# Kernel tuning notes

Measured on AMD Instinct MI355X. Metric: run time of the kernel, lower is better.

## Reference

```python
import jax, jax.numpy as jnp
import numpy as np

N = 50000
E = 800000
DIN = 256
DH = 256
DOUT = 256
R = 8
B = 4


def setup_inputs() -> dict:
    key = jax.random.key(0)
    ks = jax.random.split(key, 12)
    s = 0.05
    return {
        "x": jax.random.normal(ks[0], (N, DIN), jnp.float32),
        "edge_index": jax.random.randint(ks[1], (2, E), 0, N, jnp.int64),
        "edge_type": jax.random.randint(ks[2], (E,), 0, R, jnp.int64),
        "basis1": jax.random.normal(ks[3], (B, DIN, DH), jnp.float32) * s,
        "comp1": jax.random.normal(ks[4], (R, B), jnp.float32) * s,
        "root1": jax.random.normal(ks[5], (DIN, DH), jnp.float32) * s,
        "bias1": jnp.zeros((DH,), jnp.float32),
        "basis2": jax.random.normal(ks[6], (B, DH, DOUT), jnp.float32) * s,
        "comp2": jax.random.normal(ks[7], (R, B), jnp.float32) * s,
        "root2": jax.random.normal(ks[8], (DH, DOUT), jnp.float32) * s,
        "bias2": jnp.zeros((DOUT,), jnp.float32),
    }


def rgcn_conv(x, src, dst, edge_type, basis, comp, root, bias):
    # Basis-decomposed relational conv (PyG RGCNConv, aggr='mean').
    # xb: per-node transform by each basis matrix -> [N, B, out]
    xb = jnp.einsum('ni,bio->nbo', x, basis)
    # Per-edge message: mix bases with relation coefficients -> [E, out]
    msg = jnp.einsum('eb,ebo->eo', comp[edge_type], xb[src])
    # Mean aggregation per (dst, relation): divide each edge by the count of
    # edges of its relation arriving at its destination, then scatter-add.
    key = dst * R + edge_type
    cnt = jax.ops.segment_sum(jnp.ones((msg.shape[0],), x.dtype), key,
                              num_segments=x.shape[0] * R)
    norm = 1.0 / jnp.maximum(cnt, 1.0)
    agg = jax.ops.segment_sum(msg * norm[key][:, None], dst,
                              num_segments=x.shape[0])
    return agg + x @ root + bias


def reference(x, edge_index, edge_type, basis1, comp1, root1, bias1,
              basis2, comp2, root2, bias2):
    src, dst = edge_index[0], edge_index[1]
    h = rgcn_conv(x, src, dst, edge_type, basis1, comp1, root1, bias1)
    h = jax.nn.relu(h)
    # dropout(p=0.4) is identity in eval mode
    out = rgcn_conv(h, src, dst, edge_type, basis2, comp2, root2, bias2)
    return out
```

## Files before the change

kernel.cpp:

```cpp
#include <hip/hip_runtime.h>
#include <hip/hip_bf16.h>

constexpr int N_NODES = 50000;
constexpr int N_EDGES = 800000;
constexpr int R_REL   = 8;
constexpr int BASES   = 4;
constexpr int D       = 256;
constexpr int KT      = BASES * D + D;

typedef __attribute__((ext_vector_type(8))) short bf16x8;
typedef __attribute__((ext_vector_type(4))) float f32x4;

__device__ inline float bfu_lo(unsigned u) { return __uint_as_float(u << 16); }
__device__ inline float bfu_hi(unsigned u) { return __uint_as_float(u & 0xFFFF0000u); }
__device__ inline unsigned short f2bu(float f) {
  __hip_bfloat16 h = __float2bfloat16(f);
  return *reinterpret_cast<unsigned short*>(&h);
}
__device__ inline void store_out(float* p, float v) { *p = v; }
__device__ inline void store_out(__hip_bfloat16* p, float v) { *p = __float2bfloat16(v); }

__device__ inline void gload_lds16(void* lds, const void* g) {
  __builtin_amdgcn_global_load_lds(
      (const __attribute__((address_space(1))) unsigned*)g,
      (__attribute__((address_space(3))) unsigned*)lds, 16, 0, 0);
}

__global__ __launch_bounds__(256) void count_kernel(
    const int* __restrict__ ei, const int* __restrict__ et,
    int* __restrict__ cnt) {
  int e = blockIdx.x * 256 + threadIdx.x;
  if (e < N_EDGES) {
    int dst = ei[N_EDGES + e];
    int rt  = et[e];
    atomicAdd(&cnt[dst * R_REL + rt], 1);
  }
}

__global__ __launch_bounds__(256) void scan_phaseA(
    const int* __restrict__ cnt, int* __restrict__ bsum) {
  __shared__ int sd[256];
  int tid = threadIdx.x;
  int n = blockIdx.x * 256 + tid;
  int d = 0;
  if (n < N_NODES) {
#pragma unroll
    for (int r = 0; r < R_REL; r++) d += cnt[n * R_REL + r];
  }
  sd[tid] = d;
  __syncthreads();
  for (int off = 128; off > 0; off >>= 1) {
    if (tid < off) sd[tid] += sd[tid + off];
    __syncthreads();
  }
  if (tid == 0) bsum[blockIdx.x] = sd[0];
}

__global__ __launch_bounds__(256) void scan_phaseB(
    const int* __restrict__ bsum, int* __restrict__ boff,
    int* __restrict__ estart, int NB) {
  __shared__ int sd[256];
  int tid = threadIdx.x;
  int v = (tid < NB) ? bsum[tid] : 0;
  sd[tid] = v;
  __syncthreads();
  for (int off = 1; off < 256; off <<= 1) {
    int t = (tid >= off) ? sd[tid - off] : 0;
    __syncthreads();
    sd[tid] += t;
    __syncthreads();
  }
  if (tid < NB) boff[tid] = sd[tid] - v;
  if (tid == 0) estart[N_NODES] = N_EDGES;
}

__global__ __launch_bounds__(256) void scan_phaseC(
    const int* __restrict__ cnt, const int* __restrict__ boff,
    int* __restrict__ estart) {
  __shared__ int sd[256];
  int tid = threadIdx.x;
  int n = blockIdx.x * 256 + tid;
  int d = 0;
  if (n < N_NODES) {
#pragma unroll
    for (int r = 0; r < R_REL; r++) d += cnt[n * R_REL + r];
  }
  sd[tid] = d;
  __syncthreads();
  for (int off = 1; off < 256; off <<= 1) {
    int t = (tid >= off) ? sd[tid - off] : 0;
    __syncthreads();
    sd[tid] += t;
    __syncthreads();
  }
  if (n < N_NODES) estart[n] = boff[blockIdx.x] + sd[tid] - d;
}

__global__ __launch_bounds__(256) void bucket_kernel(
    const int* __restrict__ ei, const int* __restrict__ et,
    const int* __restrict__ estart, int* __restrict__ cursor,
    int* __restrict__ packed) {
  int e = blockIdx.x * 256 + threadIdx.x;
  if (e < N_EDGES) {
    int src = ei[e];
    int dst = ei[N_EDGES + e];
    int rt  = et[e];
    int pos = estart[dst] + atomicAdd(&cursor[dst], 1);
    packed[pos] = src | (rt << 20);
  }
}

__global__ __launch_bounds__(256) void convert_kernel(
    const float* __restrict__ x, unsigned* __restrict__ x2) {
  int idx = blockIdx.x * 256 + threadIdx.x;
  if (idx < N_NODES * 128) {
    float2 v = *(const float2*)(x + (size_t)idx * 2);
    x2[idx] = (unsigned)f2bu(v.x) | ((unsigned)f2bu(v.y) << 16);
  }
}

__global__ __launch_bounds__(256) void winv_kernel(
    const int* __restrict__ cnt, const float* __restrict__ comp,
    float4* __restrict__ wtab) {
  int idx = blockIdx.x * 256 + threadIdx.x;
  if (idx < N_NODES * R_REL) {
    int r = idx & 7;
    int c = cnt[idx];
    float inv = 1.0f / (float)(c > 0 ? c : 1);
    float4 w;
    w.x = comp[r * BASES + 0] * inv;
    w.y = comp[r * BASES + 1] * inv;
    w.z = comp[r * BASES + 2] * inv;
    w.w = comp[r * BASES + 3] * inv;
    wtab[idx] = w;
  }
}

__global__ __launch_bounds__(256) void make_w_kernel(
    const float* __restrict__ basis, const float* __restrict__ root,
    __hip_bfloat16* __restrict__ WT) {
  __shared__ __hip_bfloat16 tile[64][256];
  int k0 = blockIdx.x * 64;
  int tid = threadIdx.x;
#pragma unroll 4
  for (int r = 0; r < 64; r++) {
    int k = k0 + r;
    const float* srow = (k < BASES * D)
        ? basis + ((size_t)(k & 3) * D + (k >> 2)) * D
        : root + (size_t)(k - BASES * D) * D;
    tile[r][tid] = __float2bfloat16(srow[tid]);
  }
  __syncthreads();
  __hip_bfloat16* dst = WT + (size_t)tid * KT + k0;
#pragma unroll
  for (int c = 0; c < 8; c++) {
    union { short s[8]; int4 v; } u;
#pragma unroll
    for (int r = 0; r < 8; r++)
      u.s[r] = *reinterpret_cast<short*>(&tile[c * 8 + r][tid]);
    *(int4*)(dst + c * 8) = u.v;
  }
}

__device__ inline void edge_fma(float acc[BASES][4], uint2 v, float4 w) {
  float a0 = bfu_lo(v.x), a1 = bfu_hi(v.x), a2 = bfu_lo(v.y), a3 = bfu_hi(v.y);
  acc[0][0] += w.x * a0; acc[0][1] += w.x * a1; acc[0][2] += w.x * a2; acc[0][3] += w.x * a3;
  acc[1][0] += w.y * a0; acc[1][1] += w.y * a1; acc[1][2] += w.y * a2; acc[1][3] += w.y * a3;
  acc[2][0] += w.z * a0; acc[2][1] += w.z * a1; acc[2][2] += w.z * a2; acc[2][3] += w.z * a3;
  acc[3][0] += w.w * a0; acc[3][1] += w.w * a1; acc[3][2] += w.w * a2; acc[3][3] += w.w * a3;
}

__global__ __launch_bounds__(256) void aggregate_kernel(
    const unsigned* __restrict__ x2,
    const int* __restrict__ packed,
    const int* __restrict__ estart,
    const float4* __restrict__ wtab,
    __hip_bfloat16* __restrict__ zA)
{
  int tid = threadIdx.x;
  int wave = tid >> 6, lane = tid & 63;
  int n = blockIdx.x * 4 + wave;
  const float4 wzero = make_float4(0.f, 0.f, 0.f, 0.f);

  float acc[BASES][4] = {};
  int s = estart[n], e = estart[n + 1];
  const float4* wt = wtab + (size_t)n * R_REL;

  for (int base = s; base < e; base += 4) {
    int rem = e - base;
    int i1 = base + (rem > 1 ? 1 : 0);
    int i2 = base + (rem > 2 ? 2 : 0);
    int i3 = base + (rem > 3 ? 3 : 0);
    int p0 = packed[base];
    int p1 = packed[i1];
    int p2 = packed[i2];
    int p3 = packed[i3];
    uint2 v0 = *(const uint2*)(x2 + (size_t)(p0 & 0xFFFFF) * 128 + lane * 2);
    uint2 v1 = *(const uint2*)(x2 + (size_t)(p1 & 0xFFFFF) * 128 + lane * 2);
    uint2 v2 = *(const uint2*)(x2 + (size_t)(p2 & 0xFFFFF) * 128 + lane * 2);
    uint2 v3 = *(const uint2*)(x2 + (size_t)(p3 & 0xFFFFF) * 128 + lane * 2);
    float4 w0 = wt[p0 >> 20];
    float4 w1 = (rem > 1) ? wt[p1 >> 20] : wzero;
    float4 w2 = (rem > 2) ? wt[p2 >> 20] : wzero;
    float4 w3 = (rem > 3) ? wt[p3 >> 20] : wzero;
    edge_fma(acc, v0, w0);
    edge_fma(acc, v1, w1);
    edge_fma(acc, v2, w2);
    edge_fma(acc, v3, w3);
  }

  union { short s[8]; int4 v; } u0, u1;
#pragma unroll
  for (int j = 0; j < 2; j++)
#pragma unroll
    for (int b = 0; b < BASES; b++) {
      u0.s[4 * j + b] = (short)f2bu(acc[b][j]);
      u1.s[4 * j + b] = (short)f2bu(acc[b][j + 2]);
    }
  __hip_bfloat16* zrow = zA + (size_t)n * KT;
  *(int4*)(zrow + 16 * lane) = u0.v;
  *(int4*)(zrow + 16 * lane + 8) = u1.v;

  uint2 sv = *(const uint2*)(x2 + (size_t)n * 128 + lane * 2);
  *(uint2*)((unsigned*)(zrow + BASES * D) + lane * 2) = sv;
}

#define BM 128
#define BN 256
#define BK 32

template <bool RELU, typename OutT>
__global__ __launch_bounds__(512) void gemm_kernel(
    const __hip_bfloat16* __restrict__ A,
    const __hip_bfloat16* __restrict__ Bt,
    const float* __restrict__ bias, OutT* __restrict__ C, int M) {
  __shared__ __align__(16) __hip_bfloat16 As[BM * BK];
  __shared__ __align__(16) __hip_bfloat16 Bs[BN * BK];
  int tid = threadIdx.x;
  int m0 = blockIdx.x * BM;
  int wave = tid >> 6, lane = tid & 63;
  int wm = wave & 1, wn = wave >> 1;
  int l15 = lane & 15, quad = lane >> 4;

  int colS = (lane & 3) * 8;
  int rowA = wave * 16 + (lane >> 2);
  int grA  = min(m0 + rowA, M - 1);
  const __hip_bfloat16* gA  = A + (size_t)grA * KT + colS;
  const __hip_bfloat16* gB0 = Bt + (size_t)(wave * 32 + (lane >> 2)) * KT + colS;
  const __hip_bfloat16* gB1 = gB0 + 16 * KT;
  __hip_bfloat16* lA  = As + wave * 512;
  __hip_bfloat16* lB0 = Bs + wave * 1024;
  __hip_bfloat16* lB1 = Bs + wave * 1024 + 512;

  f32x4 acc[4][4] = {};

  for (int k0 = 0; k0 < KT; k0 += BK) {
    gload_lds16(lA, gA + k0);
    gload_lds16(lB0, gB0 + k0);
    gload_lds16(lB1, gB1 + k0);
    __syncthreads();

    bf16x8 af[4], bfr[4];
#pragma unroll
    for (int mt = 0; mt < 4; mt++)
      af[mt] = *(const bf16x8*)(As + (wm * 64 + mt * 16 + l15) * BK + quad * 8);
#pragma unroll
    for (int nt = 0; nt < 4; nt++)
      bfr[nt] = *(const bf16x8*)(Bs + (wn * 64 + nt * 16 + l15) * BK + quad * 8);
#pragma unroll
    for (int mt = 0; mt < 4; mt++)
#pragma unroll
      for (int nt = 0; nt < 4; nt++)
        acc[mt][nt] = __builtin_amdgcn_mfma_f32_16x16x32_bf16(
            af[mt], bfr[nt], acc[mt][nt], 0, 0, 0);
    __syncthreads();
  }

#pragma unroll
  for (int nt = 0; nt < 4; nt++) {
    int cg = wn * 64 + nt * 16 + l15;
    float bv = bias[cg];
#pragma unroll
    for (int mt = 0; mt < 4; mt++) {
#pragma unroll
      for (int r = 0; r < 4; r++) {
        int rg = m0 + wm * 64 + mt * 16 + quad * 4 + r;
        if (rg < M) {
          float v = acc[mt][nt][r] + bv;
          if (RELU) v = fmaxf(v, 0.f);
          store_out(C + (size_t)rg * D + cg, v);
        }
      }
    }
  }
}

static inline char* carve(char*& p, size_t bytes) {
  char* r = p;
  p += (bytes + 255) & ~(size_t)255;
  return r;
}

extern "C" void kernel_launch(void* const* d_in, const int* in_sizes, int n_in,
                              void* d_out, int out_size, void* d_ws,
                              size_t ws_size, hipStream_t stream) {
  const float* x      = (const float*)d_in[0];
  const int*   ei     = (const int*)d_in[1];
  const int*   et     = (const int*)d_in[2];
  const float* basis1 = (const float*)d_in[3];
  const float* comp1  = (const float*)d_in[4];
  const float* root1  = (const float*)d_in[5];
  const float* bias1  = (const float*)d_in[6];
  const float* basis2 = (const float*)d_in[7];
  const float* comp2  = (const float*)d_in[8];
  const float* root2  = (const float*)d_in[9];
  const float* bias2  = (const float*)d_in[10];
  float* out = (float*)d_out;

  char* ws = (char*)d_ws;
  int* cnt    = (int*)carve(ws, (size_t)N_NODES * R_REL * 4);
  int* estart = (int*)carve(ws, (size_t)(N_NODES + 1) * 4);
  int* cursor = (int*)carve(ws, (size_t)N_NODES * 4);
  int* bsum   = (int*)carve(ws, 256 * 4);
  int* boff   = (int*)carve(ws, 256 * 4);
  int* packed = (int*)carve(ws, (size_t)N_EDGES * 4);
  float4* wtab1 = (float4*)carve(ws, (size_t)N_NODES * R_REL * 16);
  float4* wtab2 = (float4*)carve(ws, (size_t)N_NODES * R_REL * 16);
  __hip_bfloat16* WT1 = (__hip_bfloat16*)carve(ws, (size_t)D * KT * 2);
  __hip_bfloat16* WT2 = (__hip_bfloat16*)carve(ws, (size_t)D * KT * 2);
  unsigned* xb = (unsigned*)carve(ws, (size_t)N_NODES * D * 2);
  __hip_bfloat16* h = (__hip_bfloat16*)carve(ws, (size_t)N_NODES * D * 2);
  __hip_bfloat16* zA = (__hip_bfloat16*)carve(ws, (size_t)N_NODES * KT * 2);

  const int NB = (N_NODES + 255) / 256;
  const int EB = (N_EDGES + 255) / 256;
  const int CB = (N_NODES * 128 + 255) / 256;
  const int WB = (N_NODES * R_REL + 255) / 256;

  hipMemsetAsync(cnt, 0, (size_t)N_NODES * R_REL * 4, stream);
  hipMemsetAsync(cursor, 0, (size_t)N_NODES * 4, stream);

  count_kernel<<<EB, 256, 0, stream>>>(ei, et, cnt);
  scan_phaseA<<<NB, 256, 0, stream>>>(cnt, bsum);
  scan_phaseB<<<1, 256, 0, stream>>>(bsum, boff, estart, NB);
  scan_phaseC<<<NB, 256, 0, stream>>>(cnt, boff, estart);
  bucket_kernel<<<EB, 256, 0, stream>>>(ei, et, estart, cursor, packed);

  convert_kernel<<<CB, 256, 0, stream>>>(x, xb);
  winv_kernel<<<WB, 256, 0, stream>>>(cnt, comp1, wtab1);
  winv_kernel<<<WB, 256, 0, stream>>>(cnt, comp2, wtab2);
  make_w_kernel<<<KT / 64, 256, 0, stream>>>(basis1, root1, WT1);
  make_w_kernel<<<KT / 64, 256, 0, stream>>>(basis2, root2, WT2);

  dim3 ggrid((N_NODES + BM - 1) / BM, 1);
  const int AB = (N_NODES + 3) / 4;

  aggregate_kernel<<<AB, 256, 0, stream>>>(xb, packed, estart, wtab1, zA);
  gemm_kernel<true, __hip_bfloat16><<<ggrid, 512, 0, stream>>>(zA, WT1, bias1, h, N_NODES);

  aggregate_kernel<<<AB, 256, 0, stream>>>((const unsigned*)h, packed, estart, wtab2, zA);
  gemm_kernel<false, float><<<ggrid, 512, 0, stream>>>(zA, WT2, bias2, out, N_NODES);
}
```

Measured before the change: 499.2 us.

## Sort edges by (dst,relation) with atomic ranks, fuse winv, retile GEMM

Edge bucketing now records each edge's atomic rank inside its (dst, relation) key and scans over all node-relation keys. This removes the second cursor atomic pass and the cursor memset, and computes both normalization tables inside the scan kernel, so two winv launches disappear. The aggregation loop processes 8 edges per iteration to put more gathers in flight. The GEMM moves to 64-row tiles with 256 threads, each wave owning a 64-column slice, which trades A-tile reuse for more blocks.

Measured after the change: 544.3 us. 9.0% more time.

```diff
diff --git a/kernel.cpp b/kernel.cpp
--- a/kernel.cpp
+++ b/kernel.cpp
@@ -7,6 +7,7 @@
 constexpr int BASES   = 4;
 constexpr int D       = 256;
 constexpr int KT      = BASES * D + D;
+constexpr int NKEYS   = N_NODES * R_REL;
 
 typedef __attribute__((ext_vector_type(8))) short bf16x8;
 typedef __attribute__((ext_vector_type(4))) float f32x4;
@@ -26,27 +27,26 @@
       (__attribute__((address_space(3))) unsigned*)lds, 16, 0, 0);
 }
 
-__global__ __launch_bounds__(256) void count_kernel(
+__global__ __launch_bounds__(256) void count_rank_kernel(
     const int* __restrict__ ei, const int* __restrict__ et,
-    int* __restrict__ cnt) {
+    int* __restrict__ cnt, int* __restrict__ rank) {
   int e = blockIdx.x * 256 + threadIdx.x;
   if (e < N_EDGES) {
     int dst = ei[N_EDGES + e];
     int rt  = et[e];
-    atomicAdd(&cnt[dst * R_REL + rt], 1);
-  }
-}
+    rank[e] = atomicAdd(&cnt[dst * R_REL + rt], 1);
+  }
+}
+
+constexpr int SCAN_B = (NKEYS + 255) / 256;
+constexpr int CHUNK  = (SCAN_B + 255) / 256;
 
 __global__ __launch_bounds__(256) void scan_phaseA(
     const int* __restrict__ cnt, int* __restrict__ bsum) {
   __shared__ int sd[256];
   int tid = threadIdx.x;
-  int n = blockIdx.x * 256 + tid;
-  int d = 0;
-  if (n < N_NODES) {
-#pragma unroll
-    for (int r = 0; r < R_REL; r++) d += cnt[n * R_REL + r];
-  }
+  int idx = blockIdx.x * 256 + tid;
+  int d = (idx < NKEYS) ? cnt[idx] : 0;
   sd[tid] = d;
   __syncthreads();
   for (int off = 128; off > 0; off >>= 1) {
@@ -58,11 +58,18 @@
 
 __global__ __launch_bounds__(256) void scan_phaseB(
     const int* __restrict__ bsum, int* __restrict__ boff,
-    int* __restrict__ estart, int NB) {
+    int* __restrict__ ecdf) {
   __shared__ int sd[256];
   int tid = threadIdx.x;
-  int v = (tid < NB) ? bsum[tid] : 0;
-  sd[tid] = v;
+  int loc[CHUNK];
+  int lsum = 0;
+#pragma unroll
+  for (int j = 0; j < CHUNK; j++) {
+    int i = tid * CHUNK + j;
+    loc[j] = (i < SCAN_B) ? bsum[i] : 0;
+    lsum += loc[j];
+  }
+  sd[tid] = lsum;
   __syncthreads();
   for (int off = 1; off < 256; off <<= 1) {
     int t = (tid >= off) ? sd[tid - off] : 0;
@@ -70,21 +77,25 @@
     sd[tid] += t;
     __syncthreads();
   }
-  if (tid < NB) boff[tid] = sd[tid] - v;
-  if (tid == 0) estart[N_NODES] = N_EDGES;
-}
-
-__global__ __launch_bounds__(256) void scan_phaseC(
+  int running = sd[tid] - lsum;
+#pragma unroll
+  for (int j = 0; j < CHUNK; j++) {
+    int i = tid * CHUNK + j;
+    if (i < SCAN_B) boff[i] = running;
+    running += loc[j];
+  }
+  if (tid == 0) ecdf[NKEYS] = N_EDGES;
+}
+
+__global__ __launch_bounds__(256) void scan_phaseC_winv(
     const int* __restrict__ cnt, const int* __restrict__ boff,
-    int* __restrict__ estart) {
+    const float* __restrict__ comp1, const float* __restrict__ comp2,
+    int* __restrict__ ecdf, float4* __restrict__ wtab1,
+    float4* __restrict__ wtab2) {
   __shared__ int sd[256];
   int tid = threadIdx.x;
-  int n = blockIdx.x * 256 + tid;
-  int d = 0;
-  if (n < N_NODES) {
-#pragma unroll
-    for (int r = 0; r < R_REL; r++) d += cnt[n * R_REL + r];
-  }
+  int idx = blockIdx.x * 256 + tid;
+  int d = (idx < NKEYS) ? cnt[idx] : 0;
   sd[tid] = d;
   __syncthreads();
   for (int off = 1; off < 256; off <<= 1) {
@@ -93,19 +104,27 @@
     sd[tid] += t;
     __syncthreads();
   }
-  if (n < N_NODES) estart[n] = boff[blockIdx.x] + sd[tid] - d;
+  if (idx < NKEYS) {
+    ecdf[idx] = boff[blockIdx.x] + sd[tid] - d;
+    int r = idx & 7;
+    float inv = 1.0f / (float)(d > 0 ? d : 1);
+    float4 c1 = *(const float4*)(comp1 + r * BASES);
+    float4 c2 = *(const float4*)(comp2 + r * BASES);
+    wtab1[idx] = make_float4(c1.x * inv, c1.y * inv, c1.z * inv, c1.w * inv);
+    wtab2[idx] = make_float4(c2.x * inv, c2.y * inv, c2.z * inv, c2.w * inv);
+  }
 }
 
 __global__ __launch_bounds__(256) void bucket_kernel(
     const int* __restrict__ ei, const int* __restrict__ et,
-    const int* __restrict__ estart, int* __restrict__ cursor,
+    const int* __restrict__ rank, const int* __restrict__ ecdf,
     int* __restrict__ packed) {
   int e = blockIdx.x * 256 + threadIdx.x;
   if (e < N_EDGES) {
     int src = ei[e];
     int dst = ei[N_EDGES + e];
     int rt  = et[e];
-    int pos = estart[dst] + atomicAdd(&cursor[dst], 1);
+    int pos = ecdf[dst * R_REL + rt] + rank[e];
     packed[pos] = src | (rt << 20);
   }
 }
@@ -116,23 +135,6 @@
   if (idx < N_NODES * 128) {
     float2 v = *(const float2*)(x + (size_t)idx * 2);
     x2[idx] = (unsigned)f2bu(v.x) | ((unsigned)f2bu(v.y) << 16);
-  }
-}
-
-__global__ __launch_bounds__(256) void winv_kernel(
-    const int* __restrict__ cnt, const float* __restrict__ comp,
-    float4* __restrict__ wtab) {
-  int idx = blockIdx.x * 256 + threadIdx.x;
-  if (idx < N_NODES * R_REL) {
-    int r = idx & 7;
-    int c = cnt[idx];
-    float inv = 1.0f / (float)(c > 0 ? c : 1);
-    float4 w;
-    w.x = comp[r * BASES + 0] * inv;
-    w.y = comp[r * BASES + 1] * inv;
-    w.z = comp[r * BASES + 2] * inv;
-    w.w = comp[r * BASES + 3] * inv;
-    wtab[idx] = w;
   }
 }
 
@@ -173,7 +175,7 @@
 __global__ __launch_bounds__(256) void aggregate_kernel(
     const unsigned* __restrict__ x2,
     const int* __restrict__ packed,
-    const int* __restrict__ estart,
+    const int* __restrict__ ecdf,
     const float4* __restrict__ wtab,
     __hip_bfloat16* __restrict__ zA)
 {
@@ -183,18 +185,31 @@
   const float4 wzero = make_float4(0.f, 0.f, 0.f, 0.f);
 
   float acc[BASES][4] = {};
-  int s = estart[n], e = estart[n + 1];
+  int s = ecdf[n * R_REL], e = ecdf[n * R_REL + R_REL];
   const float4* wt = wtab + (size_t)n * R_REL;
-
-  for (int base = s; base < e; base += 4) {
+  int base = s;
+
+  for (; base + 8 <= e; base += 8) {
+    int p[8];
+#pragma unroll
+    for (int i = 0; i < 8; i++) p[i] = packed[base + i];
+    uint2 v[8];
+#pragma unroll
+    for (int i = 0; i < 8; i++)
+      v[i] = *(const uint2*)(x2 + (size_t)(p[i] & 0xFFFFF) * 128 + lane * 2);
+    float4 w[8];
+#pragma unroll
+    for (int i = 0; i < 8; i++) w[i] = wt[p[i] >> 20];
+#pragma unroll
+    for (int i = 0; i < 8; i++) edge_fma(acc, v[i], w[i]);
+  }
+
+  for (; base < e; base += 4) {
     int rem = e - base;
     int i1 = base + (rem > 1 ? 1 : 0);
     int i2 = base + (rem > 2 ? 2 : 0);
     int i3 = base + (rem > 3 ? 3 : 0);
-    int p0 = packed[base];
-    int p1 = packed[i1];
-    int p2 = packed[i2];
-    int p3 = packed[i3];
+    int p0 = packed[base], p1 = packed[i1], p2 = packed[i2], p3 = packed[i3];
     uint2 v0 = *(const uint2*)(x2 + (size_t)(p0 & 0xFFFFF) * 128 + lane * 2);
     uint2 v1 = *(const uint2*)(x2 + (size_t)(p1 & 0xFFFFF) * 128 + lane * 2);
     uint2 v2 = *(const uint2*)(x2 + (size_t)(p2 & 0xFFFFF) * 128 + lane * 2);
@@ -225,12 +240,12 @@
   *(uint2*)((unsigned*)(zrow + BASES * D) + lane * 2) = sv;
 }
 
-#define BM 128
+#define BM 64
 #define BN 256
 #define BK 32
 
 template <bool RELU, typename OutT>
-__global__ __launch_bounds__(512) void gemm_kernel(
+__global__ __launch_bounds__(256) void gemm_kernel(
     const __hip_bfloat16* __restrict__ A,
     const __hip_bfloat16* __restrict__ Bt,
     const float* __restrict__ bias, OutT* __restrict__ C, int M) {
@@ -239,34 +254,36 @@
   int tid = threadIdx.x;
   int m0 = blockIdx.x * BM;
   int wave = tid >> 6, lane = tid & 63;
-  int wm = wave & 1, wn = wave >> 1;
   int l15 = lane & 15, quad = lane >> 4;
 
   int colS = (lane & 3) * 8;
-  int rowA = wave * 16 + (lane >> 2);
-  int grA  = min(m0 + rowA, M - 1);
-  const __hip_bfloat16* gA  = A + (size_t)grA * KT + colS;
-  const __hip_bfloat16* gB0 = Bt + (size_t)(wave * 32 + (lane >> 2)) * KT + colS;
-  const __hip_bfloat16* gB1 = gB0 + 16 * KT;
-  __hip_bfloat16* lA  = As + wave * 512;
-  __hip_bfloat16* lB0 = Bs + wave * 1024;
-  __hip_bfloat16* lB1 = Bs + wave * 1024 + 512;
+  int r16  = lane >> 2;
+  int grA  = min(m0 + wave * 16 + r16, M - 1);
+  const __hip_bfloat16* gA = A + (size_t)grA * KT + colS;
+  __hip_bfloat16* lA = As + wave * 512;
+  const __hip_bfloat16* gB[4];
+  __hip_bfloat16* lB[4];
+#pragma unroll
+  for (int c = 0; c < 4; c++) {
+    gB[c] = Bt + (size_t)(wave * 64 + c * 16 + r16) * KT + colS;
+    lB[c] = Bs + wave * 2048 + c * 512;
+  }
 
   f32x4 acc[4][4] = {};
 
   for (int k0 = 0; k0 < KT; k0 += BK) {
     gload_lds16(lA, gA + k0);
-    gload_lds16(lB0, gB0 + k0);
-    gload_lds16(lB1, gB1 + k0);
+#pragma unroll
+    for (int c = 0; c < 4; c++) gload_lds16(lB[c], gB[c] + k0);
     __syncthreads();
 
     bf16x8 af[4], bfr[4];
 #pragma unroll
     for (int mt = 0; mt < 4; mt++)
-      af[mt] = *(const bf16x8*)(As + (wm * 64 + mt * 16 + l15) * BK + quad * 8);
+      af[mt] = *(const bf16x8*)(As + (mt * 16 + l15) * BK + quad * 8);
 #pragma unroll
     for (int nt = 0; nt < 4; nt++)
-      bfr[nt] = *(const bf16x8*)(Bs + (wn * 64 + nt * 16 + l15) * BK + quad * 8);
+      bfr[nt] = *(const bf16x8*)(Bs + (wave * 64 + nt * 16 + l15) * BK + quad * 8);
 #pragma unroll
     for (int mt = 0; mt < 4; mt++)
 #pragma unroll
@@ -278,13 +295,13 @@
 
 #pragma unroll
   for (int nt = 0; nt < 4; nt++) {
-    int cg = wn * 64 + nt * 16 + l15;
+    int cg = wave * 64 + nt * 16 + l15;
     float bv = bias[cg];
 #pragma unroll
     for (int mt = 0; mt < 4; mt++) {
 #pragma unroll
       for (int r = 0; r < 4; r++) {
-        int rg = m0 + wm * 64 + mt * 16 + quad * 4 + r;
+        int rg = m0 + mt * 16 + quad * 4 + r;
         if (rg < M) {
           float v = acc[mt][nt][r] + bv;
           if (RELU) v = fmaxf(v, 0.f);
@@ -318,46 +335,42 @@
   float* out = (float*)d_out;
 
   char* ws = (char*)d_ws;
-  int* cnt    = (int*)carve(ws, (size_t)N_NODES * R_REL * 4);
-  int* estart = (int*)carve(ws, (size_t)(N_NODES + 1) * 4);
-  int* cursor = (int*)carve(ws, (size_t)N_NODES * 4);
-  int* bsum   = (int*)carve(ws, 256 * 4);
-  int* boff   = (int*)carve(ws, 256 * 4);
+  int* cnt    = (int*)carve(ws, (size_t)NKEYS * 4);
+  int* ecdf   = (int*)carve(ws, (size_t)(NKEYS + 1) * 4);
+  int* rank   = (int*)carve(ws, (size_t)N_EDGES * 4);
+  int* bsum   = (int*)carve(ws, (size_t)SCAN_B * 4);
+  int* boff   = (int*)carve(ws, (size_t)SCAN_B * 4);
   int* packed = (int*)carve(ws, (size_t)N_EDGES * 4);
-  float4* wtab1 = (float4*)carve(ws, (size_t)N_NODES * R_REL * 16);
-  float4* wtab2 = (float4*)carve(ws, (size_t)N_NODES * R_REL * 16);
+  float4* wtab1 = (float4*)carve(ws, (size_t)NKEYS * 16);
+  float4* wtab2 = (float4*)carve(ws, (size_t)NKEYS * 16);
   __hip_bfloat16* WT1 = (__hip_bfloat16*)carve(ws, (size_t)D * KT * 2);
   __hip_bfloat16* WT2 = (__hip_bfloat16*)carve(ws, (size_t)D * KT * 2);
   unsigned* xb = (unsigned*)carve(ws, (size_t)N_NODES * D * 2);
   __hip_bfloat16* h = (__hip_bfloat16*)carve(ws, (size_t)N_NODES * D * 2);
   __hip_bfloat16* zA = (__hip_bfloat16*)carve(ws, (size_t)N_NODES * KT * 2);
 
-  const int NB = (N_NODES + 255) / 256;
   const int EB = (N_EDGES + 255) / 256;
   const int CB = (N_NODES * 128 + 255) / 256;
-  const int WB = (N_NODES * R_REL + 255) / 256;
-
-  hipMemsetAsync(cnt, 0, (size_t)N_NODES * R_REL * 4, stream);
-  hipMemsetAsync(cursor, 0, (size_t)N_NODES * 4, stream);
-
-  count_kernel<<<EB, 256, 0, stream>>>(ei, et, cnt);
-  scan_phaseA<<<NB, 256, 0, stream>>>(cnt, bsum);
-  scan_phaseB<<<1, 256, 0, stream>>>(bsum, boff, estart, NB);
-  scan_phaseC<<<NB, 256, 0, stream>>>(cnt, boff, estart);
-  bucket_kernel<<<EB, 256, 0, stream>>>(ei, et, estart, cursor, packed);
+
+  hipMemsetAsync(cnt, 0, (size_t)NKEYS * 4, stream);
+
+  count_rank_kernel<<<EB, 256, 0, stream>>>(ei, et, cnt, rank);
+  scan_phaseA<<<SCAN_B, 256, 0, stream>>>(cnt, bsum);
+  scan_phaseB<<<1, 256, 0, stream>>>(bsum, boff, ecdf);
+  scan_phaseC_winv<<<SCAN_B, 256, 0, stream>>>(cnt, boff, comp1, comp2,
+                                               ecdf, wtab1, wtab2);
+  bucket_kernel<<<EB, 256, 0, stream>>>(ei, et, rank, ecdf, packed);
 
   convert_kernel<<<CB, 256, 0, stream>>>(x, xb);
-  winv_kernel<<<WB, 256, 0, stream>>>(cnt, comp1, wtab1);
-  winv_kernel<<<WB, 256, 0, stream>>>(cnt, comp2, wtab2);
   make_w_kernel<<<KT / 64, 256, 0, stream>>>(basis1, root1, WT1);
   make_w_kernel<<<KT / 64, 256, 0, stream>>>(basis2, root2, WT2);
 
-  dim3 ggrid((N_NODES + BM - 1) / BM, 1);
+  const int GB = (N_NODES + BM - 1) / BM;
   const int AB = (N_NODES + 3) / 4;
 
-  aggregate_kernel<<<AB, 256, 0, stream>>>(xb, packed, estart, wtab1, zA);
-  gemm_kernel<true, __hip_bfloat16><<<ggrid, 512, 0, stream>>>(zA, WT1, bias1, h, N_NODES);
-
-  aggregate_kernel<<<AB, 256, 0, stream>>>((const unsigned*)h, packed, estart, wtab2, zA);
-  gemm_kernel<false, float><<<ggrid, 512, 0, stream>>>(zA, WT2, bias2, out, N_NODES);
-}
+  aggregate_kernel<<<AB, 256, 0, stream>>>(xb, packed, ecdf, wtab1, zA);
+  gemm_kernel<true, __hip_bfloat16><<<GB, 256, 0, stream>>>(zA, WT1, bias1, h, N_NODES);
+
+  aggregate_kernel<<<AB, 256, 0, stream>>>((const unsigned*)h, packed, ecdf, wtab2, zA);
+  gemm_kernel<false, float><<<GB, 256, 0, stream>>>(zA, WT2, bias2, out, N_NODES);
+}
```
